# Performance work log

Measured on AMD Instinct MI355X. Metric: run time of the kernel, lower is better.

Reference implementation:

```python
import jax, jax.numpy as jnp
import numpy as np

HEAD = 16

def setup_inputs() -> dict:
    key = jax.random.key(0)
    kq, kk, kv = jax.random.split(key, 3)
    B, S, D = 2, 2048, 1024
    q = jax.random.normal(kq, (B, S, D), dtype=jnp.float32)
    k = jax.random.normal(kk, (B, S, D), dtype=jnp.float32)
    v = jax.random.normal(kv, (B, S, D), dtype=jnp.float32)
    return {"q": q, "k": k, "v": v}

def reference(q, k, v):
    # NOTE: the source module overwrites the projected q1/k1/v1 with the raw
    # inputs (q1 = q, etc.), so w_q/w_k/w_v/w_o never affect the output.
    B, S, D = q.shape
    H = HEAD
    hd = D // H
    # [B, S, D] -> [B, H, S, hd]
    qh = q.reshape(B, S, H, hd).transpose(0, 2, 1, 3)
    kh = k.reshape(B, S, H, hd).transpose(0, 2, 1, 3)
    vh = v.reshape(B, S, H, hd).transpose(0, 2, 1, 3)
    scale = 1.0 / jnp.sqrt(jnp.float32(hd))
    scores = jnp.einsum('bhqd,bhkd->bhqk', qh, kh) * scale  # [B, H, S, S]
    attn = jax.nn.softmax(scores, axis=-1)
    x = jnp.einsum('bhqk,bhkd->bhqd', attn, vh)             # [B, H, S, hd]
    return x.transpose(0, 2, 1, 3).reshape(B, S, D)
```

## Files before the change

### kernel.cpp

```cpp
#include <hip/hip_runtime.h>
#include <hip/hip_bf16.h>

typedef __attribute__((ext_vector_type(8)))  __bf16 bf16x8;
typedef __attribute__((ext_vector_type(4)))  __bf16 bf16x4;
typedef __attribute__((ext_vector_type(4)))  float  f32x4;
typedef __attribute__((ext_vector_type(16))) float  f32x16;

#define S_LEN    2048
#define D_MODEL  1024
#define NH       16
#define HD       64
#define QB       128
#define NTILE    32
#define NOUTER   16
#define C_SCALE  0.18033688011112042f

static __device__ __forceinline__ f32x16 mfma32(bf16x8 a, bf16x8 b, f32x16 c) {
    return __builtin_amdgcn_mfma_f32_32x32x16_bf16(a, b, c, 0, 0, 0);
}

static __device__ __forceinline__ void gload16(const void* g, void* l) {
    __builtin_amdgcn_global_load_lds(
        (const __attribute__((address_space(1))) void*)g,
        (__attribute__((address_space(3)))       void*)l, 16, 0, 0);
}

__global__ __launch_bounds__(256, 4)
void prep_kernel(const float* __restrict__ Kp, const float* __restrict__ Vp,
                 char* __restrict__ Kb, char* __restrict__ Vb)
{
    const int bid  = blockIdx.x;
    const int bh   = bid >> 5;
    const int tile = bid & 31;
    const int b = bh >> 4, h = bh & 15;
    const int tid = threadIdx.x;
    const size_t gbase = (size_t)b * S_LEN * D_MODEL + (size_t)h * HD;
    char* kout = Kb + (size_t)bid * 8192;
    char* vout = Vb + (size_t)bid * 8192;

    {
        const int krow = tid >> 2, c2 = tid & 3;
        const float* kp = Kp + gbase + (size_t)(tile * 64 + krow) * D_MODEL + c2 * 16;
        f32x4 x0 = *(const f32x4*)(kp);
        f32x4 x1 = *(const f32x4*)(kp + 4);
        f32x4 x2 = *(const f32x4*)(kp + 8);
        f32x4 x3 = *(const f32x4*)(kp + 12);
        bf16x8 f0, f1;
        #pragma unroll
        for (int j = 0; j < 4; ++j) {
            f0[j] = (__bf16)x0[j]; f0[j + 4] = (__bf16)x1[j];
            f1[j] = (__bf16)x2[j]; f1[j + 4] = (__bf16)x3[j];
        }
        const int sw = (krow & 7) << 4;
        *(bf16x8*)(kout + krow * 128 + ((c2 * 32)      ^ sw)) = f0;
        *(bf16x8*)(kout + krow * 128 + ((c2 * 32 + 16) ^ sw)) = f1;
    }
    {
        const int vkg = tid >> 4, vdg = tid & 15;
        const float* vp = Vp + gbase + (size_t)(tile * 64 + vkg * 4) * D_MODEL + vdg * 4;
        f32x4 r0 = *(const f32x4*)(vp);
        f32x4 r1 = *(const f32x4*)(vp + D_MODEL);
        f32x4 r2 = *(const f32x4*)(vp + 2 * D_MODEL);
        f32x4 r3 = *(const f32x4*)(vp + 3 * D_MODEL);
        const int kvoff = 8 * ((vkg >> 1) & 1) + 16 * (vkg & 1) + 32 * (vkg >> 2);
        #pragma unroll
        for (int c = 0; c < 4; ++c) {
            const int d = vdg * 4 + c;
            bf16x4 pk;
            pk[0] = (__bf16)r0[c]; pk[1] = (__bf16)r1[c];
            pk[2] = (__bf16)r2[c]; pk[3] = (__bf16)r3[c];
            *(bf16x4*)(vout + d * 128 + (kvoff ^ ((d & 7) << 4))) = pk;
        }
    }
}

__global__ __launch_bounds__(512, 4)
void attn_kernel(const float* __restrict__ Qp, const char* __restrict__ Kb,
                 const char* __restrict__ Vb, float* __restrict__ Op)
{
    __shared__ __align__(16) char smem[65536];

    const int bid = blockIdx.x;
    const int bh = bid & 31, qtile = bid >> 5;
    const int b = bh >> 4, h = bh & 15;
    const int tid = threadIdx.x;
    const int w = tid >> 6, lane = tid & 63;
    const int ql = lane & 31, hi = lane >> 5;
    const int qs = w & 3, kh = w >> 2;

    const size_t gbase = (size_t)b * S_LEN * D_MODEL + (size_t)h * HD;

    bf16x8 qf[4];
    {
        const int qrow = qtile * QB + qs * 32 + ql;
        const float* qp = Qp + gbase + (size_t)qrow * D_MODEL + hi * 8;
        #pragma unroll
        for (int ks = 0; ks < 4; ++ks) {
            f32x4 a = *(const f32x4*)(qp + ks * 16);
            f32x4 c = *(const f32x4*)(qp + ks * 16 + 4);
            bf16x8 f;
            #pragma unroll
            for (int j = 0; j < 4; ++j) {
                f[j]     = (__bf16)(a[j] * C_SCALE);
                f[j + 4] = (__bf16)(c[j] * C_SCALE);
            }
            qf[ks] = f;
        }
    }

    const char* kg0 = Kb + (size_t)(bh * NTILE) * 8192;
    const char* vg0 = Vb + (size_t)(bh * NTILE) * 8192;

    auto stage = [&](int db, int t) {
        const char* kg = kg0 + (size_t)t * 16384;
        const char* vg = vg0 + (size_t)t * 16384;
        char* kl = smem + db * 16384;
        char* vl = smem + 32768 + db * 16384;
        const int o0 = w * 2048, o1 = w * 2048 + 1024;
        gload16(kg + o0 + lane * 16, kl + o0);
        gload16(kg + o1 + lane * 16, kl + o1);
        gload16(vg + o0 + lane * 16, vl + o0);
        gload16(vg + o1 + lane * 16, vl + o1);
    };

    f32x16 oa = {0,0,0,0,0,0,0,0,0,0,0,0,0,0,0,0};
    f32x16 ob = {0,0,0,0,0,0,0,0,0,0,0,0,0,0,0,0};
    f32x4 l4 = {0.f, 0.f, 0.f, 0.f};

    auto soft = [&](const f32x16& sv, bf16x8* dst) {
        float p[16];
        #pragma unroll
        for (int i = 0; i < 16; ++i) {
            p[i] = __builtin_amdgcn_exp2f(sv[i]);
            l4[i & 3] += p[i];
        }
        #pragma unroll
        for (int z = 0; z < 2; ++z) {
            bf16x8 f;
            #pragma unroll
            for (int j = 0; j < 8; ++j) f[j] = (__bf16)p[z * 8 + j];
            dst[z] = f;
        }
    };

    stage(0, 0);
    int cur = 0;
    for (int t = 0; t < NOUTER; ++t) {
        __syncthreads();
        if (t + 1 < NOUTER) stage(cur ^ 1, t + 1);

        const char* kl = smem + cur * 16384 + kh * 8192;
        const char* vl = smem + 32768 + cur * 16384 + kh * 8192;

        f32x16 s0 = {0,0,0,0,0,0,0,0,0,0,0,0,0,0,0,0};
        f32x16 s1 = {0,0,0,0,0,0,0,0,0,0,0,0,0,0,0,0};
        __builtin_amdgcn_s_setprio(1);
        #pragma unroll
        for (int ks = 0; ks < 4; ++ks) {
            const int col = 32 * ks + 16 * hi;
            const int r0 = ql, r1 = 32 + ql;
            bf16x8 k0 = *(const bf16x8*)(kl + r0 * 128 + (col ^ ((r0 & 7) << 4)));
            bf16x8 k1 = *(const bf16x8*)(kl + r1 * 128 + (col ^ ((r1 & 7) << 4)));
            s0 = mfma32(k0, qf[ks], s0);
            s1 = mfma32(k1, qf[ks], s1);
        }
        __builtin_amdgcn_s_setprio(0);

        bf16x8 pa[4];
        soft(s0, &pa[0]);
        soft(s1, &pa[2]);

        __builtin_amdgcn_s_setprio(1);
        #pragma unroll
        for (int ks = 0; ks < 4; ++ks) {
            const int col = 32 * ks + 16 * hi;
            const int d0 = ql, d1 = 32 + ql;
            bf16x8 v0 = *(const bf16x8*)(vl + d0 * 128 + (col ^ ((d0 & 7) << 4)));
            bf16x8 v1 = *(const bf16x8*)(vl + d1 * 128 + (col ^ ((d1 & 7) << 4)));
            oa = mfma32(pa[ks], v0, oa);
            ob = mfma32(pa[ks], v1, ob);
        }
        __builtin_amdgcn_s_setprio(0);
        cur ^= 1;
    }

    float lsum = (l4[0] + l4[1]) + (l4[2] + l4[3]);
    __syncthreads();
    lsum += __shfl_xor(lsum, 32);
    float* lbuf = (float*)(smem + 32768);
    float* obuf = (float*)smem;
    if (lane < 32) lbuf[kh * 128 + qs * 32 + ql] = lsum;
    __syncthreads();
    if (kh == 1) {
        #pragma unroll
        for (int i = 0; i < 16; ++i) {
            const int qloc = (i & 3) + 8 * (i >> 2) + 4 * hi;
            obuf[qs * 2048 + qloc * 64 + ql]      = oa[i];
            obuf[qs * 2048 + qloc * 64 + 32 + ql] = ob[i];
        }
    }
    __syncthreads();
    if (kh == 0) {
        #pragma unroll
        for (int i = 0; i < 16; ++i) {
            const int qloc = (i & 3) + 8 * (i >> 2) + 4 * hi;
            const float lt = lbuf[qs * 32 + qloc] + lbuf[128 + qs * 32 + qloc];
            const float inv = 1.0f / lt;
            const float v0 = (oa[i] + obuf[qs * 2048 + qloc * 64 + ql])      * inv;
            const float v1 = (ob[i] + obuf[qs * 2048 + qloc * 64 + 32 + ql]) * inv;
            float* op = Op + gbase + (size_t)(qtile * QB + qs * 32 + qloc) * D_MODEL;
            op[ql]      = v0;
            op[32 + ql] = v1;
        }
    }
}

extern "C" void kernel_launch(void* const* d_in, const int* in_sizes, int n_in,
                              void* d_out, int out_size, void* d_ws, size_t ws_size,
                              hipStream_t stream) {
    const float* q = (const float*)d_in[0];
    const float* k = (const float*)d_in[1];
    const float* v = (const float*)d_in[2];
    float* out = (float*)d_out;
    char* Kb = (char*)d_ws;
    char* Vb = (char*)d_ws + 8 * 1024 * 1024;

    prep_kernel<<<dim3(32 * NTILE), dim3(256), 0, stream>>>(k, v, Kb, Vb);
    attn_kernel<<<dim3(32 * (S_LEN / QB)), dim3(512), 0, stream>>>(q, Kb, Vb, out);
}
```

Baseline: 57.50 us.

## Halve attention block to 4 warps, each computing two 32-row query sub-tiles

Shrinks the attention block from 8 to 4 waves. Each wave now owns 64 query rows (two 32-row sub-tiles) instead of 32, so every K and V fragment read from LDS feeds twice as many MFMAs. This cuts LDS read traffic per FLOP and puts more independent MFMA chains in flight per wave. In exchange it doubles accumulator and score registers per wave, which adds register pressure, and lowers the number of waves available to hide latency (launch bounds 256,2).

```diff
diff --git a/kernel.cpp b/kernel.cpp
--- a/kernel.cpp
+++ b/kernel.cpp
@@ -74,7 +74,7 @@
     }
 }
 
-__global__ __launch_bounds__(512, 4)
+__global__ __launch_bounds__(256, 2)
 void attn_kernel(const float* __restrict__ Qp, const char* __restrict__ Kb,
                  const char* __restrict__ Vb, float* __restrict__ Op)
 {
@@ -86,25 +86,26 @@
     const int tid = threadIdx.x;
     const int w = tid >> 6, lane = tid & 63;
     const int ql = lane & 31, hi = lane >> 5;
-    const int qs = w & 3, kh = w >> 2;
+    const int qp = w & 1, kh = w >> 1;
 
     const size_t gbase = (size_t)b * S_LEN * D_MODEL + (size_t)h * HD;
 
-    bf16x8 qf[4];
-    {
-        const int qrow = qtile * QB + qs * 32 + ql;
-        const float* qp = Qp + gbase + (size_t)qrow * D_MODEL + hi * 8;
+    bf16x8 qf[2][4];
+    #pragma unroll
+    for (int sub = 0; sub < 2; ++sub) {
+        const int qrow = qtile * QB + qp * 64 + sub * 32 + ql;
+        const float* qp_ = Qp + gbase + (size_t)qrow * D_MODEL + hi * 8;
         #pragma unroll
         for (int ks = 0; ks < 4; ++ks) {
-            f32x4 a = *(const f32x4*)(qp + ks * 16);
-            f32x4 c = *(const f32x4*)(qp + ks * 16 + 4);
+            f32x4 a = *(const f32x4*)(qp_ + ks * 16);
+            f32x4 c = *(const f32x4*)(qp_ + ks * 16 + 4);
             bf16x8 f;
             #pragma unroll
             for (int j = 0; j < 4; ++j) {
                 f[j]     = (__bf16)(a[j] * C_SCALE);
                 f[j + 4] = (__bf16)(c[j] * C_SCALE);
             }
-            qf[ks] = f;
+            qf[sub][ks] = f;
         }
     }
 
@@ -116,23 +117,27 @@
         const char* vg = vg0 + (size_t)t * 16384;
         char* kl = smem + db * 16384;
         char* vl = smem + 32768 + db * 16384;
-        const int o0 = w * 2048, o1 = w * 2048 + 1024;
-        gload16(kg + o0 + lane * 16, kl + o0);
-        gload16(kg + o1 + lane * 16, kl + o1);
-        gload16(vg + o0 + lane * 16, vl + o0);
-        gload16(vg + o1 + lane * 16, vl + o1);
+        #pragma unroll
+        for (int j = 0; j < 4; ++j) {
+            const int o = j * 4096 + tid * 16;
+            gload16(kg + o, kl + o);
+            gload16(vg + o, vl + o);
+        }
     };
 
-    f32x16 oa = {0,0,0,0,0,0,0,0,0,0,0,0,0,0,0,0};
-    f32x16 ob = {0,0,0,0,0,0,0,0,0,0,0,0,0,0,0,0};
-    f32x4 l4 = {0.f, 0.f, 0.f, 0.f};
-
-    auto soft = [&](const f32x16& sv, bf16x8* dst) {
+    f32x16 oa0 = {0,0,0,0,0,0,0,0,0,0,0,0,0,0,0,0};
+    f32x16 ob0 = {0,0,0,0,0,0,0,0,0,0,0,0,0,0,0,0};
+    f32x16 oa1 = {0,0,0,0,0,0,0,0,0,0,0,0,0,0,0,0};
+    f32x16 ob1 = {0,0,0,0,0,0,0,0,0,0,0,0,0,0,0,0};
+    f32x4 l4a = {0.f, 0.f, 0.f, 0.f};
+    f32x4 l4b = {0.f, 0.f, 0.f, 0.f};
+
+    auto soft = [](const f32x16& sv, bf16x8* dst, f32x4& lacc) {
         float p[16];
         #pragma unroll
         for (int i = 0; i < 16; ++i) {
             p[i] = __builtin_amdgcn_exp2f(sv[i]);
-            l4[i & 3] += p[i];
+            lacc[i & 3] += p[i];
         }
         #pragma unroll
         for (int z = 0; z < 2; ++z) {
@@ -152,8 +157,10 @@
         const char* kl = smem + cur * 16384 + kh * 8192;
         const char* vl = smem + 32768 + cur * 16384 + kh * 8192;
 
-        f32x16 s0 = {0,0,0,0,0,0,0,0,0,0,0,0,0,0,0,0};
-        f32x16 s1 = {0,0,0,0,0,0,0,0,0,0,0,0,0,0,0,0};
+        f32x16 s00 = {0,0,0,0,0,0,0,0,0,0,0,0,0,0,0,0};
+        f32x16 s01 = {0,0,0,0,0,0,0,0,0,0,0,0,0,0,0,0};
+        f32x16 s10 = {0,0,0,0,0,0,0,0,0,0,0,0,0,0,0,0};
+        f32x16 s11 = {0,0,0,0,0,0,0,0,0,0,0,0,0,0,0,0};
         __builtin_amdgcn_s_setprio(1);
         #pragma unroll
         for (int ks = 0; ks < 4; ++ks) {
@@ -161,14 +168,18 @@
             const int r0 = ql, r1 = 32 + ql;
             bf16x8 k0 = *(const bf16x8*)(kl + r0 * 128 + (col ^ ((r0 & 7) << 4)));
             bf16x8 k1 = *(const bf16x8*)(kl + r1 * 128 + (col ^ ((r1 & 7) << 4)));
-            s0 = mfma32(k0, qf[ks], s0);
-            s1 = mfma32(k1, qf[ks], s1);
+            s00 = mfma32(k0, qf[0][ks], s00);
+            s01 = mfma32(k1, qf[0][ks], s01);
+            s10 = mfma32(k0, qf[1][ks], s10);
+            s11 = mfma32(k1, qf[1][ks], s11);
         }
         __builtin_amdgcn_s_setprio(0);
 
-        bf16x8 pa[4];
-        soft(s0, &pa[0]);
-        soft(s1, &pa[2]);
+        bf16x8 pa0[4], pa1[4];
+        soft(s00, &pa0[0], l4a);
+        soft(s01, &pa0[2], l4a);
+        soft(s10, &pa1[0], l4b);
+        soft(s11, &pa1[2], l4b);
 
         __builtin_amdgcn_s_setprio(1);
         #pragma unroll
@@ -177,26 +188,36 @@
             const int d0 = ql, d1 = 32 + ql;
             bf16x8 v0 = *(const bf16x8*)(vl + d0 * 128 + (col ^ ((d0 & 7) << 4)));
             bf16x8 v1 = *(const bf16x8*)(vl + d1 * 128 + (col ^ ((d1 & 7) << 4)));
-            oa = mfma32(pa[ks], v0, oa);
-            ob = mfma32(pa[ks], v1, ob);
+            oa0 = mfma32(pa0[ks], v0, oa0);
+            ob0 = mfma32(pa0[ks], v1, ob0);
+            oa1 = mfma32(pa1[ks], v0, oa1);
+            ob1 = mfma32(pa1[ks], v1, ob1);
         }
         __builtin_amdgcn_s_setprio(0);
         cur ^= 1;
     }
 
-    float lsum = (l4[0] + l4[1]) + (l4[2] + l4[3]);
+    float lsA = (l4a[0] + l4a[1]) + (l4a[2] + l4a[3]);
+    float lsB = (l4b[0] + l4b[1]) + (l4b[2] + l4b[3]);
+    lsA += __shfl_xor(lsA, 32);
+    lsB += __shfl_xor(lsB, 32);
     __syncthreads();
-    lsum += __shfl_xor(lsum, 32);
     float* lbuf = (float*)(smem + 32768);
     float* obuf = (float*)smem;
-    if (lane < 32) lbuf[kh * 128 + qs * 32 + ql] = lsum;
+    const int qs0 = qp * 2, qs1 = qp * 2 + 1;
+    if (lane < 32) {
+        lbuf[kh * 128 + qs0 * 32 + ql] = lsA;
+        lbuf[kh * 128 + qs1 * 32 + ql] = lsB;
+    }
     __syncthreads();
     if (kh == 1) {
         #pragma unroll
         for (int i = 0; i < 16; ++i) {
             const int qloc = (i & 3) + 8 * (i >> 2) + 4 * hi;
-            obuf[qs * 2048 + qloc * 64 + ql]      = oa[i];
-            obuf[qs * 2048 + qloc * 64 + 32 + ql] = ob[i];
+            obuf[qs0 * 2048 + qloc * 64 + ql]      = oa0[i];
+            obuf[qs0 * 2048 + qloc * 64 + 32 + ql] = ob0[i];
+            obuf[qs1 * 2048 + qloc * 64 + ql]      = oa1[i];
+            obuf[qs1 * 2048 + qloc * 64 + 32 + ql] = ob1[i];
         }
     }
     __syncthreads();
@@ -204,13 +225,16 @@
         #pragma unroll
         for (int i = 0; i < 16; ++i) {
             const int qloc = (i & 3) + 8 * (i >> 2) + 4 * hi;
-            const float lt = lbuf[qs * 32 + qloc] + lbuf[128 + qs * 32 + qloc];
-            const float inv = 1.0f / lt;
-            const float v0 = (oa[i] + obuf[qs * 2048 + qloc * 64 + ql])      * inv;
-            const float v1 = (ob[i] + obuf[qs * 2048 + qloc * 64 + 32 + ql]) * inv;
-            float* op = Op + gbase + (size_t)(qtile * QB + qs * 32 + qloc) * D_MODEL;
-            op[ql]      = v0;
-            op[32 + ql] = v1;
+            const float ltA = lbuf[qs0 * 32 + qloc] + lbuf[128 + qs0 * 32 + qloc];
+            const float ltB = lbuf[qs1 * 32 + qloc] + lbuf[128 + qs1 * 32 + qloc];
+            const float invA = 1.0f / ltA;
+            const float invB = 1.0f / ltB;
+            float* opA = Op + gbase + (size_t)(qtile * QB + qs0 * 32 + qloc) * D_MODEL;
+            float* opB = Op + gbase + (size_t)(qtile * QB + qs1 * 32 + qloc) * D_MODEL;
+            opA[ql]      = (oa0[i] + obuf[qs0 * 2048 + qloc * 64 + ql])      * invA;
+            opA[32 + ql] = (ob0[i] + obuf[qs0 * 2048 + qloc * 64 + 32 + ql]) * invA;
+            opB[ql]      = (oa1[i] + obuf[qs1 * 2048 + qloc * 64 + ql])      * invB;
+            opB[32 + ql] = (ob1[i] + obuf[qs1 * 2048 + qloc * 64 + 32 + ql]) * invB;
         }
     }
 }
@@ -226,5 +250,5 @@
     char* Vb = (char*)d_ws + 8 * 1024 * 1024;
 
     prep_kernel<<<dim3(32 * NTILE), dim3(256), 0, stream>>>(k, v, Kb, Vb);
-    attn_kernel<<<dim3(32 * (S_LEN / QB)), dim3(512), 0, stream>>>(q, Kb, Vb, out);
-}
+    attn_kernel<<<dim3(32 * (S_LEN / QB)), dim3(256), 0, stream>>>(q, Kb, Vb, out);
+}
```

After: 58.05 us. No clear change (+0.9%).
